# Kernel optimization log

Measured on AMD Instinct MI355X. Metric: run time of the kernel, lower is better.

## Reference

```python
import jax, jax.numpy as jnp
import numpy as np

N = 50000      # nodes
E = 400000     # edges
CIN = 15
HID = 128
HEADS = 4
NC = 2
EPS_BN = 1e-5


def _bn(x, g, b, m, v):
    # BatchNorm1d in eval mode: running stats
    return g * (x - m) * jax.lax.rsqrt(v + EPS_BN) + b


def _gat(x, src, dst, w, a_s, a_d, bias):
    # PyG GATConv(heads=4, concat=False): adds self-loops, per-head attention,
    # softmax over incoming edges (grouped by dst), mean over heads + bias.
    sl = jnp.arange(N, dtype=src.dtype)
    src = jnp.concatenate([src, sl]); dst = jnp.concatenate([dst, sl])
    h = (x @ w).reshape(N, HEADS, HID)                     # [N,H,C]
    a_src = jnp.einsum('nhc,hc->nh', h, a_s)               # [N,H]
    a_dst = jnp.einsum('nhc,hc->nh', h, a_d)
    e = jax.nn.leaky_relu(a_src[src] + a_dst[dst], 0.2)    # [E',H]
    m = jax.ops.segment_max(e, dst, num_segments=N)        # stable segment softmax
    ex = jnp.exp(e - m[dst])
    s = jax.ops.segment_sum(ex, dst, num_segments=N)
    alpha = ex / (s[dst] + 1e-16)
    out = jax.ops.segment_sum(alpha[:, :, None] * h[src], dst, num_segments=N)
    return out.mean(axis=1) + bias                         # concat=False -> head mean


def _gcn(x, src, dst, ew, w, bias):
    # PyG GCNConv with edge_weight: self-loops (weight 1), symmetric normalization.
    sl = jnp.arange(N, dtype=src.dtype)
    src_f = jnp.concatenate([src, sl]); dst_f = jnp.concatenate([dst, sl])
    ew_f = jnp.concatenate([ew, jnp.ones((N,), ew.dtype)])
    deg = jax.ops.segment_sum(ew_f, dst_f, num_segments=N)
    dinv = jnp.where(deg > 0, jax.lax.rsqrt(jnp.maximum(deg, 1e-12)), 0.0)
    norm = dinv[src_f] * ew_f * dinv[dst_f]
    h = x @ w
    return jax.ops.segment_sum(norm[:, None] * h[src_f], dst_f, num_segments=N) + bias


def setup_inputs() -> dict:
    key = jax.random.key(0)
    ks = iter(jax.random.split(key, 40))
    nrm = lambda s, sc: jax.random.normal(next(ks), s, jnp.float32) * sc
    H2 = HID // 2
    inp = {
        'x': jax.random.normal(next(ks), (N, CIN), jnp.float32),
        'edge_index': jax.random.randint(next(ks), (2, E), 0, N, jnp.int32),
        'edge_attr': jax.random.uniform(next(ks), (E, 1), jnp.float32),
        # GATConv params
        'w_gat': nrm((CIN, HEADS * HID), 0.25),
        'att_src': nrm((HEADS, HID), 0.1),
        'att_dst': nrm((HEADS, HID), 0.1),
        'b_gat': jnp.zeros((HID,), jnp.float32),
        # GCNConv params
        'w2': nrm((HID, HID), 0.09), 'b2': jnp.zeros((HID,), jnp.float32),
        'w3': nrm((HID, HID), 0.09), 'b3': jnp.zeros((HID,), jnp.float32),
        'w4': nrm((HID, HID), 0.09), 'b4': jnp.zeros((HID,), jnp.float32),
        # BatchNorm (4 layers stacked): gamma, beta, running_mean, running_var
        'bn_g': 1.0 + nrm((4, HID), 0.1),
        'bn_b': nrm((4, HID), 0.1),
        'bn_m': nrm((4, HID), 0.1),
        'bn_v': 1.0 + 0.1 * jax.random.uniform(next(ks), (4, HID), jnp.float32),
        # dense heads
        'w_shared': nrm((HID, HID), 0.09), 'b_shared': jnp.zeros((HID,), jnp.float32),
        'w_mask1': nrm((HID, H2), 0.09), 'b_mask1': jnp.zeros((H2,), jnp.float32),
        'w_mask2': nrm((H2, NC), 0.12), 'b_mask2': jnp.zeros((NC,), jnp.float32),
        'w_inst1': nrm((HID, H2), 0.09), 'b_inst1': jnp.zeros((H2,), jnp.float32),
        'w_inst2': nrm((H2, NC), 0.12), 'b_inst2': jnp.zeros((NC,), jnp.float32),
        'w_edge1': nrm((HID, H2), 0.09), 'b_edge1': jnp.zeros((H2,), jnp.float32),
        'w_edge2': nrm((H2, 1), 0.12), 'b_edge2': jnp.zeros((1,), jnp.float32),
    }
    return inp


def reference(x, edge_index, edge_attr, w_gat, att_src, att_dst, b_gat,
              w2, b2, w3, b3, w4, b4, bn_g, bn_b, bn_m, bn_v,
              w_shared, b_shared, w_mask1, b_mask1, w_mask2, b_mask2,
              w_inst1, b_inst1, w_inst2, b_inst2, w_edge1, b_edge1, w_edge2, b_edge2):
    src, dst = edge_index[0], edge_index[1]
    ew = edge_attr.squeeze(-1)
    h = jax.nn.relu(_bn(_gat(x, src, dst, w_gat, att_src, att_dst, b_gat),
                        bn_g[0], bn_b[0], bn_m[0], bn_v[0]))
    h = jax.nn.relu(_bn(_gcn(h, src, dst, ew, w2, b2), bn_g[1], bn_b[1], bn_m[1], bn_v[1]))
    h = jax.nn.relu(_bn(_gcn(h, src, dst, ew, w3, b3), bn_g[2], bn_b[2], bn_m[2], bn_v[2]))
    h = jax.nn.relu(_bn(_gcn(h, src, dst, ew, w4, b4), bn_g[3], bn_b[3], bn_m[3], bn_v[3]))
    hs = jax.nn.relu(h @ w_shared + b_shared)
    hm = jax.nn.relu(hs @ w_mask1 + b_mask1)
    mask_out = hm @ w_mask2 + b_mask2
    hi = jax.nn.relu(hs @ w_inst1 + b_inst1)
    instance_out = hi @ w_inst2 + b_inst2
    he = jax.nn.relu(hs @ w_edge1 + b_edge1)
    edge_out = he @ w_edge2 + b_edge2
    return (mask_out, instance_out, edge_out)
```

## Files before the change

kernel.cpp:

```cpp
#include <hip/hip_runtime.h>
#include <hip/hip_bf16.h>

#define NNODES 50000
#define NEDGES 400000
#define ETOT   (NEDGES + NNODES)
#define CIN    15
#define HID    128
#define HEADS  4
#define EPS_BN 1e-5f
#define NB_SCAN ((NNODES + 255) / 256)

typedef __attribute__((ext_vector_type(8))) short bf16x8_t;
typedef __attribute__((ext_vector_type(4))) float f32x4_t;

__device__ __forceinline__ float bfu(unsigned short u) {
  return __uint_as_float(((unsigned)u) << 16);
}
__device__ __forceinline__ unsigned short f2bf(float x) {
  union { __hip_bfloat16 b; unsigned short u; } c;
  c.b = __float2bfloat16(x);
  return c.u;
}
__device__ __forceinline__ float lrelu02(float x) {
  return x > 0.0f ? x : 0.2f * x;
}

template <int WPT, int KT, int ROWS, int FUSEH>
__global__ __launch_bounds__(256) void gemm_mfma_kernel(
    const float* __restrict__ A, const unsigned short* __restrict__ WTh,
    const unsigned short* __restrict__ WTl, const float* __restrict__ bias,
    const float* __restrict__ bg, const float* __restrict__ bb,
    const float* __restrict__ bm, const float* __restrict__ bv,
    void* __restrict__ Cout, int act, int obf16,
    const float* __restrict__ w_m2, const float* __restrict__ b_m2,
    const float* __restrict__ w_i2, const float* __restrict__ b_i2,
    const float* __restrict__ w_e2, const float* __restrict__ b_e2) {
  constexpr int NC = WPT * 64;
  constexpr int RT = ROWS / 16;
  constexpr int CST = NC + 4;
  constexpr int CPR = KT / 8;
  constexpr int ABYTES = ROWS * KT * 2 * 2;
  constexpr int CBYTES = ROWS * CST * 4;
  constexpr int SBYTES = (ABYTES > CBYTES) ? ABYTES : CBYTES;
  __shared__ __align__(16) char smem[SBYTES];
  unsigned short* Ah = (unsigned short*)smem;
  unsigned short* Al = Ah + ROWS * KT;
  float* Cs = (float*)smem;

  const int tid = threadIdx.x;
  const int bm_ = blockIdx.x * ROWS;
  const int wv = tid >> 6, l = tid & 63;
  const int lcol = l & 15;
  const int kg = (l >> 4) << 3;
  const int colbase = wv * (WPT * 16);

#pragma unroll
  for (int i = 0; i < (ROWS * CPR) / 256; ++i) {
    int cch = tid + 256 * i;
    int r = cch / CPR, k0 = (cch % CPR) << 3;
    int gr = bm_ + r;
    float v[8];
    if (gr < NNODES) {
      float4 v0 = *(const float4*)&A[(size_t)gr * KT + k0];
      float4 v1 = *(const float4*)&A[(size_t)gr * KT + k0 + 4];
      v[0] = v0.x; v[1] = v0.y; v[2] = v0.z; v[3] = v0.w;
      v[4] = v1.x; v[5] = v1.y; v[6] = v1.z; v[7] = v1.w;
    } else {
#pragma unroll
      for (int j = 0; j < 8; ++j) v[j] = 0.0f;
    }
    bf16x8_t hv, lv;
#pragma unroll
    for (int j = 0; j < 8; ++j) {
      unsigned short h = f2bf(v[j]);
      hv[j] = (short)h;
      lv[j] = (short)f2bf(v[j] - bfu(h));
    }
    int byte = (k0 << 1) ^ ((r & 7) << 4);
    *(bf16x8_t*)((char*)(Ah + r * KT) + byte) = hv;
    *(bf16x8_t*)((char*)(Al + r * KT) + byte) = lv;
  }
  __syncthreads();

  f32x4_t acc[RT][WPT];
#pragma unroll
  for (int rt = 0; rt < RT; ++rt)
#pragma unroll
    for (int jj = 0; jj < WPT; ++jj) acc[rt][jj] = (f32x4_t){0.f, 0.f, 0.f, 0.f};

#pragma unroll
  for (int kc = 0; kc < KT / 32; ++kc) {
    bf16x8_t cbh[WPT], cbl[WPT];
#pragma unroll
    for (int jj = 0; jj < WPT; ++jj) {
      size_t boff = (size_t)(colbase + jj * 16 + lcol) * KT + kc * 32 + kg;
      cbh[jj] = *(const bf16x8_t*)(WTh + boff);
      cbl[jj] = *(const bf16x8_t*)(WTl + boff);
    }
    int k = kc * 32 + kg;
#pragma unroll
    for (int rt = 0; rt < RT; ++rt) {
      int lrow = rt * 16 + (l & 15);
      int byte = (k << 1) ^ ((lrow & 7) << 4);
      bf16x8_t ah = *(const bf16x8_t*)((const char*)(Ah + lrow * KT) + byte);
      bf16x8_t al = *(const bf16x8_t*)((const char*)(Al + lrow * KT) + byte);
#pragma unroll
      for (int jj = 0; jj < WPT; ++jj) {
        acc[rt][jj] = __builtin_amdgcn_mfma_f32_16x16x32_bf16(ah, cbh[jj], acc[rt][jj], 0, 0, 0);
        acc[rt][jj] = __builtin_amdgcn_mfma_f32_16x16x32_bf16(ah, cbl[jj], acc[rt][jj], 0, 0, 0);
        acc[rt][jj] = __builtin_amdgcn_mfma_f32_16x16x32_bf16(al, cbh[jj], acc[rt][jj], 0, 0, 0);
      }
    }
  }

  __syncthreads();
#pragma unroll
  for (int rt = 0; rt < RT; ++rt) {
    int trow0 = rt * 16 + ((l >> 4) << 2);
#pragma unroll
    for (int jj = 0; jj < WPT; ++jj) {
      int col = colbase + jj * 16 + lcol;
      float bs = bias ? bias[col] : 0.0f;
#pragma unroll
      for (int r = 0; r < 4; ++r) {
        float vv = acc[rt][jj][r] + bs;
        if (bg) vv = bg[col] * (vv - bm[col]) * rsqrtf(bv[col] + EPS_BN) + bb[col];
        if (act) vv = fmaxf(vv, 0.0f);
        Cs[(trow0 + r) * CST + col] = vv;
      }
    }
  }
  __syncthreads();

  if (FUSEH) {
    int r = tid >> 2, q = tid & 3;
    int grow = bm_ + r;
    const float* row = &Cs[r * CST];
    float p0 = 0.f, p1 = 0.f, p2 = 0.f, p3 = 0.f, p4 = 0.f;
#pragma unroll
    for (int e = 0; e < 16; ++e) {
      int c = q * 16 + e;
      float hm = row[c], hi = row[64 + c], he = row[128 + c];
      p0 += hm * w_m2[c * 2 + 0];
      p1 += hm * w_m2[c * 2 + 1];
      p2 += hi * w_i2[c * 2 + 0];
      p3 += hi * w_i2[c * 2 + 1];
      p4 += he * w_e2[c];
    }
#pragma unroll
    for (int off = 1; off < 4; off <<= 1) {
      p0 += __shfl_xor(p0, off);
      p1 += __shfl_xor(p1, off);
      p2 += __shfl_xor(p2, off);
      p3 += __shfl_xor(p3, off);
      p4 += __shfl_xor(p4, off);
    }
    if (q == 0 && grow < NNODES) {
      float* out = (float*)Cout;
      out[grow * 2 + 0] = p0 + b_m2[0];
      out[grow * 2 + 1] = p1 + b_m2[1];
      out[2 * NNODES + grow * 2 + 0] = p2 + b_i2[0];
      out[2 * NNODES + grow * 2 + 1] = p3 + b_i2[1];
      out[4 * NNODES + grow] = p4 + b_e2[0];
    }
  } else {
    constexpr int NJ = (ROWS * NC) / 1024;
#pragma unroll
    for (int j = 0; j < NJ; ++j) {
      int f = tid * 4 + j * 1024;
      int r = f / NC, c = f - r * NC;
      int grow = bm_ + r;
      if (grow >= NNODES) continue;
      float4 v = *(const float4*)&Cs[r * CST + c];
      if (obf16) {
        ushort4 us;
        us.x = f2bf(v.x); us.y = f2bf(v.y); us.z = f2bf(v.z); us.w = f2bf(v.w);
        *(ushort4*)&((unsigned short*)Cout)[(size_t)grow * NC + c] = us;
      } else {
        *(float4*)&((float*)Cout)[(size_t)grow * NC + c] = v;
      }
    }
  }
}

__global__ void prep_att_kernel(const float* __restrict__ w,
                                const float* __restrict__ att_s,
                                const float* __restrict__ att_d,
                                float* __restrict__ wv_s,
                                float* __restrict__ wv_d) {
  int t = threadIdx.x;
  if (t >= 60) return;
  int k = t / 4, h = t & 3;
  float s = 0.f, d = 0.f;
  for (int c = 0; c < 128; ++c) {
    float wk = w[(size_t)k * 512 + h * 128 + c];
    s += wk * att_s[h * 128 + c];
    d += wk * att_d[h * 128 + c];
  }
  wv_s[k * 4 + h] = s;
  wv_d[k * 4 + h] = d;
}

__global__ void pack_wtp_kernel(const float* __restrict__ w,
                                unsigned short* __restrict__ WTh,
                                unsigned short* __restrict__ WTl) {
  int i = blockIdx.x * blockDim.x + threadIdx.x;
  if (i >= 128 * 64) return;
  int c = i >> 6, j = i & 63;
  float xv = 0.f;
  if (j < 60) {
    int h = j / 15, k = j - h * 15;
    xv = 0.25f * w[(size_t)k * 512 + h * 128 + c];
  }
  unsigned short hh = f2bf(xv);
  WTh[i] = hh;
  WTl[i] = f2bf(xv - bfu(hh));
}

__global__ __launch_bounds__(256) void a_sd_kernel(
    const float* __restrict__ x, const float* __restrict__ wv_s,
    const float* __restrict__ wv_d, float* __restrict__ a_s,
    float* __restrict__ a_d) {
  __shared__ float xs[256 * 15];
  __shared__ float wvs[60], wvd[60];
  int t = threadIdx.x;
  int base = blockIdx.x * 256;
  if (t < 60) { wvs[t] = wv_s[t]; wvd[t] = wv_d[t]; }
  for (int i = t; i < 256 * 15; i += 256) {
    int gi = base * 15 + i;
    xs[i] = (gi < NNODES * 15) ? x[gi] : 0.0f;
  }
  __syncthreads();
  int n = base + t;
  if (n >= NNODES) return;
  float a0 = 0, a1 = 0, a2 = 0, a3 = 0, d0 = 0, d1 = 0, d2 = 0, d3 = 0;
#pragma unroll
  for (int k = 0; k < 15; ++k) {
    float xv = xs[t * 15 + k];
    a0 += xv * wvs[k * 4 + 0]; a1 += xv * wvs[k * 4 + 1];
    a2 += xv * wvs[k * 4 + 2]; a3 += xv * wvs[k * 4 + 3];
    d0 += xv * wvd[k * 4 + 0]; d1 += xv * wvd[k * 4 + 1];
    d2 += xv * wvd[k * 4 + 2]; d3 += xv * wvd[k * 4 + 3];
  }
  float4 A; A.x = a0; A.y = a1; A.z = a2; A.w = a3;
  float4 D; D.x = d0; D.y = d1; D.z = d2; D.w = d3;
  *(float4*)&a_s[n * 4] = A;
  *(float4*)&a_d[n * 4] = D;
}

__global__ __launch_bounds__(256) void gat_fused_kernel(
    const float* __restrict__ x, const float* __restrict__ a_s,
    const float* __restrict__ a_d, const int* __restrict__ rowptr,
    const int* __restrict__ csr_src, float* __restrict__ g) {
  int wid = threadIdx.x >> 6, lane = threadIdx.x & 63;
  int n = blockIdx.x * 4 + wid;
  if (n >= NNODES) return;
  int e0 = rowptr[n], e1 = rowptr[n + 1];
  bool on = lane < 60;
  int h = on ? (lane / 15) : 0;
  int k = on ? (lane - h * 15) : 0;
  float adn = a_d[n * 4 + h];

  float ssum = 0.f, acc = 0.f;
  int e = e0;
  for (; e + 4 <= e1; e += 4) {
    int s0 = csr_src[e + 0], s1 = csr_src[e + 1];
    int s2 = csr_src[e + 2], s3 = csr_src[e + 3];
    float as0 = a_s[s0 * 4 + h], as1 = a_s[s1 * 4 + h];
    float as2 = a_s[s2 * 4 + h], as3 = a_s[s3 * 4 + h];
    float x0 = x[(size_t)s0 * CIN + k], x1 = x[(size_t)s1 * CIN + k];
    float x2 = x[(size_t)s2 * CIN + k], x3 = x[(size_t)s3 * CIN + k];
    float ex0 = __expf(lrelu02(as0 + adn));
    float ex1 = __expf(lrelu02(as1 + adn));
    float ex2 = __expf(lrelu02(as2 + adn));
    float ex3 = __expf(lrelu02(as3 + adn));
    ssum += (ex0 + ex1) + (ex2 + ex3);
    acc += ex0 * x0 + ex1 * x1 + ex2 * x2 + ex3 * x3;
  }
  for (; e < e1; ++e) {
    int s = csr_src[e];
    float ex = __expf(lrelu02(a_s[s * 4 + h] + adn));
    ssum += ex;
    acc += ex * x[(size_t)s * CIN + k];
  }
  g[(size_t)n * 64 + lane] = on ? acc / (ssum + 1e-16f) : 0.0f;
}

__global__ void pack_wt4_kernel(
    const float* __restrict__ w2, const float* __restrict__ w3,
    const float* __restrict__ w4, const float* __restrict__ ws,
    unsigned short* __restrict__ Hbase, unsigned short* __restrict__ Lbase) {
  int i = blockIdx.x * blockDim.x + threadIdx.x;
  if (i >= 128 * 128) return;
  const float* W = (blockIdx.y == 0) ? w2 : (blockIdx.y == 1) ? w3
                 : (blockIdx.y == 2) ? w4 : ws;
  unsigned short* Wh = Hbase + (size_t)blockIdx.y * 128 * 128;
  unsigned short* Wl = Lbase + (size_t)blockIdx.y * 128 * 128;
  int k = i >> 7, n = i & 127;
  float x = W[i];
  unsigned short h = f2bf(x);
  Wh[n * 128 + k] = h;
  Wl[n * 128 + k] = f2bf(x - bfu(h));
}

__global__ void pack_wt192_kernel(
    const float* __restrict__ w_m1, const float* __restrict__ w_i1,
    const float* __restrict__ w_e1, const float* __restrict__ b_m1,
    const float* __restrict__ b_i1, const float* __restrict__ b_e1,
    unsigned short* __restrict__ WTh, unsigned short* __restrict__ WTl,
    float* __restrict__ b192) {
  int i = blockIdx.x * blockDim.x + threadIdx.x;
  if (i < 192 * 128) {
    int n = i >> 7, k = i & 127;
    float x = (n < 64) ? w_m1[k * 64 + n]
            : (n < 128) ? w_i1[k * 64 + (n - 64)]
                        : w_e1[k * 64 + (n - 128)];
    unsigned short h = f2bf(x);
    WTh[(size_t)n * 128 + k] = h;
    WTl[(size_t)n * 128 + k] = f2bf(x - bfu(h));
  }
  if (i < 192) {
    b192[i] = (i < 64) ? b_m1[i] : (i < 128) ? b_i1[i - 64] : b_e1[i - 128];
  }
}

__global__ void count_deg_kernel(const int* __restrict__ ei,
                                 const float* __restrict__ ea,
                                 int* __restrict__ cnt,
                                 float* __restrict__ deg) {
  int i = blockIdx.x * blockDim.x + threadIdx.x;
  if (i >= ETOT) return;
  int d; float w;
  if (i < NEDGES) { d = ei[NEDGES + i]; w = ea[i]; }
  else            { d = i - NEDGES; w = 1.0f; }
  atomicAdd(&cnt[d], 1);
  atomicAdd(&deg[d], w);
}

__global__ __launch_bounds__(256) void csr_reduce_kernel(
    const int* __restrict__ cnt, int* __restrict__ bsum) {
  __shared__ int red[256];
  int t = threadIdx.x;
  int i = blockIdx.x * 256 + t;
  red[t] = (i < NNODES) ? cnt[i] : 0;
  __syncthreads();
  for (int off = 128; off > 0; off >>= 1) {
    if (t < off) red[t] += red[t + off];
    __syncthreads();
  }
  if (t == 0) bsum[blockIdx.x] = red[0];
}

__global__ __launch_bounds__(256) void csr_scanb_kernel(
    const int* __restrict__ bsum, int* __restrict__ boff) {
  __shared__ int s[256];
  int t = threadIdx.x;
  s[t] = (t < NB_SCAN) ? bsum[t] : 0;
  __syncthreads();
  for (int off = 1; off < 256; off <<= 1) {
    int u = (t >= off) ? s[t - off] : 0;
    __syncthreads();
    s[t] += u;
    __syncthreads();
  }
  if (t < NB_SCAN) boff[t] = (t == 0) ? 0 : s[t - 1];
}

__global__ __launch_bounds__(256) void csr_scan_kernel(
    int* __restrict__ cnt, const int* __restrict__ boff,
    int* __restrict__ rowptr) {
  __shared__ int s[256];
  int t = threadIdx.x;
  int i = blockIdx.x * 256 + t;
  int v = (i < NNODES) ? cnt[i] : 0;
  s[t] = v;
  __syncthreads();
  for (int off = 1; off < 256; off <<= 1) {
    int u = (t >= off) ? s[t - off] : 0;
    __syncthreads();
    s[t] += u;
    __syncthreads();
  }
  if (i < NNODES) {
    rowptr[i] = boff[blockIdx.x] + s[t] - v;
    cnt[i] = 0;
  }
  if (i == 0) rowptr[NNODES] = ETOT;
}

__global__ void dinv_kernel(const float* __restrict__ deg,
                            float* __restrict__ dinv) {
  int n = blockIdx.x * blockDim.x + threadIdx.x;
  if (n >= NNODES) return;
  float s = deg[n];
  dinv[n] = (s > 0.0f) ? rsqrtf(fmaxf(s, 1e-12f)) : 0.0f;
}

__global__ void scatter_kernel(const int* __restrict__ ei,
                               const float* __restrict__ ea,
                               const float* __restrict__ dinv,
                               const int* __restrict__ rowptr,
                               int* __restrict__ cursor,
                               int* __restrict__ csr_src,
                               float* __restrict__ csr_ew) {
  int i = blockIdx.x * blockDim.x + threadIdx.x;
  if (i >= ETOT) return;
  int s, d; float w;
  if (i < NEDGES) { s = ei[i]; d = ei[NEDGES + i]; w = ea[i]; }
  else            { s = d = i - NEDGES; w = 1.0f; }
  int pos = rowptr[d] + atomicAdd(&cursor[d], 1);
  csr_src[pos] = s;
  csr_ew[pos] = dinv[s] * w * dinv[d];
}

__global__ __launch_bounds__(256) void gcn_gather_kernel(
    const __hip_bfloat16* __restrict__ h, const int* __restrict__ rowptr,
    const int* __restrict__ csr_src, const float* __restrict__ csr_w,
    const float* __restrict__ bias,
    const float* __restrict__ bg, const float* __restrict__ bb,
    const float* __restrict__ bm, const float* __restrict__ bv,
    float* __restrict__ out) {
  int wid = threadIdx.x >> 6, lane = threadIdx.x & 63;
  int n = blockIdx.x * 4 + wid;
  if (n >= NNODES) return;
  int e0 = rowptr[n], e1 = rowptr[n + 1];
  int c = 2 * lane;
  float ax = 0.f, ay = 0.f;
  int e = e0;
  for (; e + 4 <= e1; e += 4) {
    int s0 = csr_src[e + 0], s1 = csr_src[e + 1];
    int s2 = csr_src[e + 2], s3 = csr_src[e + 3];
    float w0 = csr_w[e + 0], w1 = csr_w[e + 1];
    float w2 = csr_w[e + 2], w3 = csr_w[e + 3];
    ushort2 u0 = *(const ushort2*)(h + (size_t)s0 * HID + c);
    ushort2 u1 = *(const ushort2*)(h + (size_t)s1 * HID + c);
    ushort2 u2 = *(const ushort2*)(h + (size_t)s2 * HID + c);
    ushort2 u3 = *(const ushort2*)(h + (size_t)s3 * HID + c);
    ax += w0 * bfu(u0.x) + w1 * bfu(u1.x) + w2 * bfu(u2.x) + w3 * bfu(u3.x);
    ay += w0 * bfu(u0.y) + w1 * bfu(u1.y) + w2 * bfu(u2.y) + w3 * bfu(u3.y);
  }
  for (; e < e1; ++e) {
    int s = csr_src[e];
    float w = csr_w[e];
    ushort2 u = *(const ushort2*)(h + (size_t)s * HID + c);
    ax += w * bfu(u.x);
    ay += w * bfu(u.y);
  }
  float ox = ax + bias[c];
  float oy = ay + bias[c + 1];
  ox = bg[c] * (ox - bm[c]) * rsqrtf(bv[c] + EPS_BN) + bb[c];
  oy = bg[c + 1] * (oy - bm[c + 1]) * rsqrtf(bv[c + 1] + EPS_BN) + bb[c + 1];
  ox = fmaxf(ox, 0.0f); oy = fmaxf(oy, 0.0f);
  float2 o; o.x = ox; o.y = oy;
  *(float2*)&out[(size_t)n * HID + c] = o;
}

extern "C" void kernel_launch(void* const* d_in, const int* in_sizes, int n_in,
                              void* d_out, int out_size, void* d_ws, size_t ws_size,
                              hipStream_t stream) {
  const float* x       = (const float*)d_in[0];
  const int*   ei      = (const int*)d_in[1];
  const float* ea      = (const float*)d_in[2];
  const float* w_gat   = (const float*)d_in[3];
  const float* att_src = (const float*)d_in[4];
  const float* att_dst = (const float*)d_in[5];
  const float* b_gat   = (const float*)d_in[6];
  const float* w2 = (const float*)d_in[7];  const float* b2 = (const float*)d_in[8];
  const float* w3 = (const float*)d_in[9];  const float* b3 = (const float*)d_in[10];
  const float* w4 = (const float*)d_in[11]; const float* b4 = (const float*)d_in[12];
  const float* bn_g = (const float*)d_in[13];
  const float* bn_b = (const float*)d_in[14];
  const float* bn_m = (const float*)d_in[15];
  const float* bn_v = (const float*)d_in[16];
  const float* w_shared = (const float*)d_in[17]; const float* b_shared = (const float*)d_in[18];
  const float* w_m1 = (const float*)d_in[19]; const float* b_m1 = (const float*)d_in[20];
  const float* w_m2 = (const float*)d_in[21]; const float* b_m2 = (const float*)d_in[22];
  const float* w_i1 = (const float*)d_in[23]; const float* b_i1 = (const float*)d_in[24];
  const float* w_i2 = (const float*)d_in[25]; const float* b_i2 = (const float*)d_in[26];
  const float* w_e1 = (const float*)d_in[27]; const float* b_e1 = (const float*)d_in[28];
  const float* w_e2 = (const float*)d_in[29]; const float* b_e2 = (const float*)d_in[30];
  float* out = (float*)d_out;

  size_t off = 0;
  auto alloc = [&](size_t bytes) -> char* {
    char* p = (char*)d_ws + off;
    off += (bytes + 255) & ~(size_t)255;
    return p;
  };
  float* p0      = (float*)alloc((size_t)NNODES * HID * 4);
  float* p1      = (float*)alloc((size_t)NNODES * HID * 4);
  float* g       = (float*)alloc((size_t)NNODES * 64 * 4);
  __hip_bfloat16* hb = (__hip_bfloat16*)alloc((size_t)NNODES * HID * 2);
  float* a_s     = (float*)alloc((size_t)NNODES * 4 * 4);
  float* a_d     = (float*)alloc((size_t)NNODES * 4 * 4);
  float* deg     = (float*)alloc((size_t)NNODES * 4);
  float* dinv    = (float*)alloc((size_t)NNODES * 4);
  float* csr_ew  = (float*)alloc((size_t)ETOT * 4);
  int*   rowptr  = (int*)alloc((size_t)(NNODES + 1) * 4);
  int*   cnt     = (int*)alloc((size_t)NNODES * 4);
  int*   csr_src = (int*)alloc((size_t)ETOT * 4);
  int*   bsum    = (int*)alloc((size_t)NB_SCAN * 4);
  int*   boff    = (int*)alloc((size_t)NB_SCAN * 4);
  unsigned short* wtH = (unsigned short*)alloc(4 * 128 * 128 * 2);
  unsigned short* wtL = (unsigned short*)alloc(4 * 128 * 128 * 2);
  unsigned short* wt192h = (unsigned short*)alloc(192 * 128 * 2);
  unsigned short* wt192l = (unsigned short*)alloc(192 * 128 * 2);
  unsigned short* wtph = (unsigned short*)alloc(128 * 64 * 2);
  unsigned short* wtpl = (unsigned short*)alloc(128 * 64 * 2);
  float* b192 = (float*)alloc(192 * 4);
  float* wv_s = (float*)alloc(60 * 4);
  float* wv_d = (float*)alloc(60 * 4);

  unsigned short* wt2h = wtH + 0 * 16384; unsigned short* wt2l = wtL + 0 * 16384;
  unsigned short* wt3h = wtH + 1 * 16384; unsigned short* wt3l = wtL + 1 * 16384;
  unsigned short* wt4h = wtH + 2 * 16384; unsigned short* wt4l = wtL + 2 * 16384;
  unsigned short* wsh  = wtH + 3 * 16384; unsigned short* wsl  = wtL + 3 * 16384;

  dim3 blk256(256);
  dim3 wgrid((NNODES + 3) / 4);
  dim3 mgrid((NNODES + 63) / 64);

  hipMemsetAsync(cnt, 0, NNODES * 4, stream);
  hipMemsetAsync(deg, 0, NNODES * 4, stream);
  count_deg_kernel<<<(ETOT + 255) / 256, blk256, 0, stream>>>(ei, ea, cnt, deg);
  csr_reduce_kernel<<<NB_SCAN, blk256, 0, stream>>>(cnt, bsum);
  csr_scanb_kernel<<<1, blk256, 0, stream>>>(bsum, boff);
  csr_scan_kernel<<<NB_SCAN, blk256, 0, stream>>>(cnt, boff, rowptr);
  dinv_kernel<<<(NNODES + 255) / 256, blk256, 0, stream>>>(deg, dinv);
  scatter_kernel<<<(ETOT + 255) / 256, blk256, 0, stream>>>(
      ei, ea, dinv, rowptr, cnt, csr_src, csr_ew);

  prep_att_kernel<<<1, 64, 0, stream>>>(w_gat, att_src, att_dst, wv_s, wv_d);
  pack_wtp_kernel<<<(128 * 64 + 255) / 256, blk256, 0, stream>>>(w_gat, wtph, wtpl);
  pack_wt4_kernel<<<dim3((128 * 128 + 255) / 256, 4), blk256, 0, stream>>>(
      w2, w3, w4, w_shared, wtH, wtL);
  pack_wt192_kernel<<<(192 * 128 + 255) / 256, blk256, 0, stream>>>(
      w_m1, w_i1, w_e1, b_m1, b_i1, b_e1, wt192h, wt192l, b192);

  a_sd_kernel<<<NB_SCAN, blk256, 0, stream>>>(x, wv_s, wv_d, a_s, a_d);

  gat_fused_kernel<<<wgrid, blk256, 0, stream>>>(
      x, a_s, a_d, rowptr, csr_src, g);

  gemm_mfma_kernel<2, 64, 64, 0><<<mgrid, blk256, 0, stream>>>(
      g, wtph, wtpl, b_gat, bn_g + 0, bn_b + 0, bn_m + 0, bn_v + 0, p0, 1, 0,
      nullptr, nullptr, nullptr, nullptr, nullptr, nullptr);

  gemm_mfma_kernel<2, 128, 64, 0><<<mgrid, blk256, 0, stream>>>(
      p0, wt2h, wt2l, nullptr, nullptr, nullptr, nullptr, nullptr, hb, 0, 1,
      nullptr, nullptr, nullptr, nullptr, nullptr, nullptr);
  gcn_gather_kernel<<<wgrid, blk256, 0, stream>>>(
      hb, rowptr, csr_src, csr_ew, b2,
      bn_g + 128, bn_b + 128, bn_m + 128, bn_v + 128, p1);

  gemm_mfma_kernel<2, 128, 64, 0><<<mgrid, blk256, 0, stream>>>(
      p1, wt3h, wt3l, nullptr, nullptr, nullptr, nullptr, nullptr, hb, 0, 1,
      nullptr, nullptr, nullptr, nullptr, nullptr, nullptr);
  gcn_gather_kernel<<<wgrid, blk256, 0, stream>>>(
      hb, rowptr, csr_src, csr_ew, b3,
      bn_g + 256, bn_b + 256, bn_m + 256, bn_v + 256, p0);

  gemm_mfma_kernel<2, 128, 64, 0><<<mgrid, blk256, 0, stream>>>(
      p0, wt4h, wt4l, nullptr, nullptr, nullptr, nullptr, nullptr, hb, 0, 1,
      nullptr, nullptr, nullptr, nullptr, nullptr, nullptr);
  gcn_gather_kernel<<<wgrid, blk256, 0, stream>>>(
      hb, rowptr, csr_src, csr_ew, b4,
      bn_g + 384, bn_b + 384, bn_m + 384, bn_v + 384, p1);

  gemm_mfma_kernel<2, 128, 64, 0><<<mgrid, blk256, 0, stream>>>(
      p1, wsh, wsl, b_shared, nullptr, nullptr, nullptr, nullptr, p0, 1, 0,
      nullptr, nullptr, nullptr, nullptr, nullptr, nullptr);

  gemm_mfma_kernel<3, 128, 64, 1><<<mgrid, blk256, 0, stream>>>(
      p0, wt192h, wt192l, b192, nullptr, nullptr, nullptr, nullptr, out, 1, 0,
      w_m2, b_m2, w_i2, b_i2, w_e2, b_e2);
}
```

Baseline: 334.1 us.

## Store activations pre-split into bf16 hi/lo planes, load GEMM A directly

Producers (GAT aggregation, GCN gather, GEMM epilogues) now write activations as two bf16 planes (high and residual) instead of fp32. The GEMM reads its A fragments straight from global memory in MFMA layout, removing the LDS staging, the per-block fp32-to-bf16 split and one barrier. Activation buffers are padded to a multiple of 64 rows so the unguarded loads stay in bounds. Padded rows are never written, so the GEMM reads uninitialised data there, although those rows are never stored. Global A loads are less coalesced than the old LDS path and may be re-fetched across the four waves.

```diff
diff --git a/kernel.cpp b/kernel.cpp
--- a/kernel.cpp
+++ b/kernel.cpp
@@ -2,6 +2,7 @@
 #include <hip/hip_bf16.h>
 
 #define NNODES 50000
+#define NPAD   50048
 #define NEDGES 400000
 #define ETOT   (NEDGES + NNODES)
 #define CIN    15
@@ -25,66 +26,31 @@
   return x > 0.0f ? x : 0.2f * x;
 }
 
-template <int WPT, int KT, int ROWS, int FUSEH>
+template <int WPT, int KT, int FUSEH>
 __global__ __launch_bounds__(256) void gemm_mfma_kernel(
-    const float* __restrict__ A, const unsigned short* __restrict__ WTh,
-    const unsigned short* __restrict__ WTl, const float* __restrict__ bias,
+    const unsigned short* __restrict__ Ahg, const unsigned short* __restrict__ Alg,
+    const unsigned short* __restrict__ WTh, const unsigned short* __restrict__ WTl,
+    const float* __restrict__ bias,
     const float* __restrict__ bg, const float* __restrict__ bb,
     const float* __restrict__ bm, const float* __restrict__ bv,
-    void* __restrict__ Cout, int act, int obf16,
+    void* __restrict__ CoutA, void* __restrict__ CoutB, int act, int omode,
     const float* __restrict__ w_m2, const float* __restrict__ b_m2,
     const float* __restrict__ w_i2, const float* __restrict__ b_i2,
     const float* __restrict__ w_e2, const float* __restrict__ b_e2) {
   constexpr int NC = WPT * 64;
-  constexpr int RT = ROWS / 16;
   constexpr int CST = NC + 4;
-  constexpr int CPR = KT / 8;
-  constexpr int ABYTES = ROWS * KT * 2 * 2;
-  constexpr int CBYTES = ROWS * CST * 4;
-  constexpr int SBYTES = (ABYTES > CBYTES) ? ABYTES : CBYTES;
-  __shared__ __align__(16) char smem[SBYTES];
-  unsigned short* Ah = (unsigned short*)smem;
-  unsigned short* Al = Ah + ROWS * KT;
-  float* Cs = (float*)smem;
+  __shared__ __align__(16) float Cs[64 * CST];
 
   const int tid = threadIdx.x;
-  const int bm_ = blockIdx.x * ROWS;
+  const int bm_ = blockIdx.x * 64;
   const int wv = tid >> 6, l = tid & 63;
   const int lcol = l & 15;
   const int kg = (l >> 4) << 3;
   const int colbase = wv * (WPT * 16);
 
-#pragma unroll
-  for (int i = 0; i < (ROWS * CPR) / 256; ++i) {
-    int cch = tid + 256 * i;
-    int r = cch / CPR, k0 = (cch % CPR) << 3;
-    int gr = bm_ + r;
-    float v[8];
-    if (gr < NNODES) {
-      float4 v0 = *(const float4*)&A[(size_t)gr * KT + k0];
-      float4 v1 = *(const float4*)&A[(size_t)gr * KT + k0 + 4];
-      v[0] = v0.x; v[1] = v0.y; v[2] = v0.z; v[3] = v0.w;
-      v[4] = v1.x; v[5] = v1.y; v[6] = v1.z; v[7] = v1.w;
-    } else {
-#pragma unroll
-      for (int j = 0; j < 8; ++j) v[j] = 0.0f;
-    }
-    bf16x8_t hv, lv;
-#pragma unroll
-    for (int j = 0; j < 8; ++j) {
-      unsigned short h = f2bf(v[j]);
-      hv[j] = (short)h;
-      lv[j] = (short)f2bf(v[j] - bfu(h));
-    }
-    int byte = (k0 << 1) ^ ((r & 7) << 4);
-    *(bf16x8_t*)((char*)(Ah + r * KT) + byte) = hv;
-    *(bf16x8_t*)((char*)(Al + r * KT) + byte) = lv;
-  }
-  __syncthreads();
-
-  f32x4_t acc[RT][WPT];
-#pragma unroll
-  for (int rt = 0; rt < RT; ++rt)
+  f32x4_t acc[4][WPT];
+#pragma unroll
+  for (int rt = 0; rt < 4; ++rt)
 #pragma unroll
     for (int jj = 0; jj < WPT; ++jj) acc[rt][jj] = (f32x4_t){0.f, 0.f, 0.f, 0.f};
 
@@ -97,13 +63,11 @@
       cbh[jj] = *(const bf16x8_t*)(WTh + boff);
       cbl[jj] = *(const bf16x8_t*)(WTl + boff);
     }
-    int k = kc * 32 + kg;
-#pragma unroll
-    for (int rt = 0; rt < RT; ++rt) {
-      int lrow = rt * 16 + (l & 15);
-      int byte = (k << 1) ^ ((lrow & 7) << 4);
-      bf16x8_t ah = *(const bf16x8_t*)((const char*)(Ah + lrow * KT) + byte);
-      bf16x8_t al = *(const bf16x8_t*)((const char*)(Al + lrow * KT) + byte);
+#pragma unroll
+    for (int rt = 0; rt < 4; ++rt) {
+      size_t aoff = (size_t)(bm_ + rt * 16 + (l & 15)) * KT + kc * 32 + kg;
+      bf16x8_t ah = *(const bf16x8_t*)(Ahg + aoff);
+      bf16x8_t al = *(const bf16x8_t*)(Alg + aoff);
 #pragma unroll
       for (int jj = 0; jj < WPT; ++jj) {
         acc[rt][jj] = __builtin_amdgcn_mfma_f32_16x16x32_bf16(ah, cbh[jj], acc[rt][jj], 0, 0, 0);
@@ -113,9 +77,8 @@
     }
   }
 
-  __syncthreads();
-#pragma unroll
-  for (int rt = 0; rt < RT; ++rt) {
+#pragma unroll
+  for (int rt = 0; rt < 4; ++rt) {
     int trow0 = rt * 16 + ((l >> 4) << 2);
 #pragma unroll
     for (int jj = 0; jj < WPT; ++jj) {
@@ -156,7 +119,7 @@
       p4 += __shfl_xor(p4, off);
     }
     if (q == 0 && grow < NNODES) {
-      float* out = (float*)Cout;
+      float* out = (float*)CoutA;
       out[grow * 2 + 0] = p0 + b_m2[0];
       out[grow * 2 + 1] = p1 + b_m2[1];
       out[2 * NNODES + grow * 2 + 0] = p2 + b_i2[0];
@@ -164,7 +127,7 @@
       out[4 * NNODES + grow] = p4 + b_e2[0];
     }
   } else {
-    constexpr int NJ = (ROWS * NC) / 1024;
+    constexpr int NJ = (64 * NC) / 1024;
 #pragma unroll
     for (int j = 0; j < NJ; ++j) {
       int f = tid * 4 + j * 1024;
@@ -172,12 +135,16 @@
       int grow = bm_ + r;
       if (grow >= NNODES) continue;
       float4 v = *(const float4*)&Cs[r * CST + c];
-      if (obf16) {
-        ushort4 us;
-        us.x = f2bf(v.x); us.y = f2bf(v.y); us.z = f2bf(v.z); us.w = f2bf(v.w);
-        *(ushort4*)&((unsigned short*)Cout)[(size_t)grow * NC + c] = us;
-      } else {
-        *(float4*)&((float*)Cout)[(size_t)grow * NC + c] = v;
+      ushort4 hi4;
+      hi4.x = f2bf(v.x); hi4.y = f2bf(v.y); hi4.z = f2bf(v.z); hi4.w = f2bf(v.w);
+      *(ushort4*)&((unsigned short*)CoutA)[(size_t)grow * NC + c] = hi4;
+      if (omode == 2) {
+        ushort4 lo4;
+        lo4.x = f2bf(v.x - bfu(hi4.x));
+        lo4.y = f2bf(v.y - bfu(hi4.y));
+        lo4.z = f2bf(v.z - bfu(hi4.z));
+        lo4.w = f2bf(v.w - bfu(hi4.w));
+        *(ushort4*)&((unsigned short*)CoutB)[(size_t)grow * NC + c] = lo4;
       }
     }
   }
@@ -251,7 +218,8 @@
 __global__ __launch_bounds__(256) void gat_fused_kernel(
     const float* __restrict__ x, const float* __restrict__ a_s,
     const float* __restrict__ a_d, const int* __restrict__ rowptr,
-    const int* __restrict__ csr_src, float* __restrict__ g) {
+    const int* __restrict__ csr_src, unsigned short* __restrict__ gh,
+    unsigned short* __restrict__ gl) {
   int wid = threadIdx.x >> 6, lane = threadIdx.x & 63;
   int n = blockIdx.x * 4 + wid;
   if (n >= NNODES) return;
@@ -283,7 +251,10 @@
     ssum += ex;
     acc += ex * x[(size_t)s * CIN + k];
   }
-  g[(size_t)n * 64 + lane] = on ? acc / (ssum + 1e-16f) : 0.0f;
+  float v = on ? acc / (ssum + 1e-16f) : 0.0f;
+  unsigned short hv = f2bf(v);
+  gh[(size_t)n * 64 + lane] = hv;
+  gl[(size_t)n * 64 + lane] = f2bf(v - bfu(hv));
 }
 
 __global__ void pack_wt4_kernel(
@@ -419,7 +390,7 @@
     const float* __restrict__ bias,
     const float* __restrict__ bg, const float* __restrict__ bb,
     const float* __restrict__ bm, const float* __restrict__ bv,
-    float* __restrict__ out) {
+    unsigned short* __restrict__ outh, unsigned short* __restrict__ outl) {
   int wid = threadIdx.x >> 6, lane = threadIdx.x & 63;
   int n = blockIdx.x * 4 + wid;
   if (n >= NNODES) return;
@@ -451,8 +422,12 @@
   ox = bg[c] * (ox - bm[c]) * rsqrtf(bv[c] + EPS_BN) + bb[c];
   oy = bg[c + 1] * (oy - bm[c + 1]) * rsqrtf(bv[c + 1] + EPS_BN) + bb[c + 1];
   ox = fmaxf(ox, 0.0f); oy = fmaxf(oy, 0.0f);
-  float2 o; o.x = ox; o.y = oy;
-  *(float2*)&out[(size_t)n * HID + c] = o;
+  ushort2 hi2, lo2;
+  hi2.x = f2bf(ox); hi2.y = f2bf(oy);
+  lo2.x = f2bf(ox - bfu(hi2.x));
+  lo2.y = f2bf(oy - bfu(hi2.y));
+  *(ushort2*)&outh[(size_t)n * HID + c] = hi2;
+  *(ushort2*)&outl[(size_t)n * HID + c] = lo2;
 }
 
 extern "C" void kernel_launch(void* const* d_in, const int* in_sizes, int n_in,
@@ -487,10 +462,13 @@
     off += (bytes + 255) & ~(size_t)255;
     return p;
   };
-  float* p0      = (float*)alloc((size_t)NNODES * HID * 4);
-  float* p1      = (float*)alloc((size_t)NNODES * HID * 4);
-  float* g       = (float*)alloc((size_t)NNODES * 64 * 4);
-  __hip_bfloat16* hb = (__hip_bfloat16*)alloc((size_t)NNODES * HID * 2);
+  unsigned short* p0h = (unsigned short*)alloc((size_t)NPAD * HID * 2);
+  unsigned short* p0l = (unsigned short*)alloc((size_t)NPAD * HID * 2);
+  unsigned short* p1h = (unsigned short*)alloc((size_t)NPAD * HID * 2);
+  unsigned short* p1l = (unsigned short*)alloc((size_t)NPAD * HID * 2);
+  unsigned short* gh  = (unsigned short*)alloc((size_t)NPAD * 64 * 2);
+  unsigned short* gl  = (unsigned short*)alloc((size_t)NPAD * 64 * 2);
+  __hip_bfloat16* hb  = (__hip_bfloat16*)alloc((size_t)NPAD * HID * 2);
   float* a_s     = (float*)alloc((size_t)NNODES * 4 * 4);
   float* a_d     = (float*)alloc((size_t)NNODES * 4 * 4);
   float* deg     = (float*)alloc((size_t)NNODES * 4);
@@ -540,38 +518,38 @@
   a_sd_kernel<<<NB_SCAN, blk256, 0, stream>>>(x, wv_s, wv_d, a_s, a_d);
 
   gat_fused_kernel<<<wgrid, blk256, 0, stream>>>(
-      x, a_s, a_d, rowptr, csr_src, g);
-
-  gemm_mfma_kernel<2, 64, 64, 0><<<mgrid, blk256, 0, stream>>>(
-      g, wtph, wtpl, b_gat, bn_g + 0, bn_b + 0, bn_m + 0, bn_v + 0, p0, 1, 0,
-      nullptr, nullptr, nullptr, nullptr, nullptr, nullptr);
-
-  gemm_mfma_kernel<2, 128, 64, 0><<<mgrid, blk256, 0, stream>>>(
-      p0, wt2h, wt2l, nullptr, nullptr, nullptr, nullptr, nullptr, hb, 0, 1,
-      nullptr, nullptr, nullptr, nullptr, nullptr, nullptr);
+      x, a_s, a_d, rowptr, csr_src, gh, gl);
+
+  gemm_mfma_kernel<2, 64, 0><<<mgrid, blk256, 0, stream>>>(
+      gh, gl, wtph, wtpl, b_gat, bn_g + 0, bn_b + 0, bn_m + 0, bn_v + 0,
+      p0h, p0l, 1, 2, nullptr, nullptr, nullptr, nullptr, nullptr, nullptr);
+
+  gemm_mfma_kernel<2, 128, 0><<<mgrid, blk256, 0, stream>>>(
+      p0h, p0l, wt2h, wt2l, nullptr, nullptr, nullptr, nullptr, nullptr,
+      hb, nullptr, 0, 1, nullptr, nullptr, nullptr, nullptr, nullptr, nullptr);
   gcn_gather_kernel<<<wgrid, blk256, 0, stream>>>(
       hb, rowptr, csr_src, csr_ew, b2,
-      bn_g + 128, bn_b + 128, bn_m + 128, bn_v + 128, p1);
-
-  gemm_mfma_kernel<2, 128, 64, 0><<<mgrid, blk256, 0, stream>>>(
-      p1, wt3h, wt3l, nullptr, nullptr, nullptr, nullptr, nullptr, hb, 0, 1,
-      nullptr, nullptr, nullptr, nullptr, nullptr, nullptr);
+      bn_g + 128, bn_b + 128, bn_m + 128, bn_v + 128, p1h, p1l);
+
+  gemm_mfma_kernel<2, 128, 0><<<mgrid, blk256, 0, stream>>>(
+      p1h, p1l, wt3h, wt3l, nullptr, nullptr, nullptr, nullptr, nullptr,
+      hb, nullptr, 0, 1, nullptr, nullptr, nullptr, nullptr, nullptr, nullptr);
   gcn_gather_kernel<<<wgrid, blk256, 0, stream>>>(
       hb, rowptr, csr_src, csr_ew, b3,
-      bn_g + 256, bn_b + 256, bn_m + 256, bn_v + 256, p0);
-
-  gemm_mfma_kernel<2, 128, 64, 0><<<mgrid, blk256, 0, stream>>>(
-      p0, wt4h, wt4l, nullptr, nullptr, nullptr, nullptr, nullptr, hb, 0, 1,
-      nullptr, nullptr, nullptr, nullptr, nullptr, nullptr);
+      bn_g + 256, bn_b + 256, bn_m + 256, bn_v + 256, p0h, p0l);
+
+  gemm_mfma_kernel<2, 128, 0><<<mgrid, blk256, 0, stream>>>(
+      p0h, p0l, wt4h, wt4l, nullptr, nullptr, nullptr, nullptr, nullptr,
+      hb, nullptr, 0, 1, nullptr, nullptr, nullptr, nullptr, nullptr, nullptr);
   gcn_gather_kernel<<<wgrid, blk256, 0, stream>>>(
       hb, rowptr, csr_src, csr_ew, b4,
-      bn_g + 384, bn_b + 384, bn_m + 384, bn_v + 384, p1);
-
-  gemm_mfma_kernel<2, 128, 64, 0><<<mgrid, blk256, 0, stream>>>(
-      p1, wsh, wsl, b_shared, nullptr, nullptr, nullptr, nullptr, p0, 1, 0,
-      nullptr, nullptr, nullptr, nullptr, nullptr, nullptr);
-
-  gemm_mfma_kernel<3, 128, 64, 1><<<mgrid, blk256, 0, stream>>>(
-      p0, wt192h, wt192l, b192, nullptr, nullptr, nullptr, nullptr, out, 1, 0,
-      w_m2, b_m2, w_i2, b_i2, w_e2, b_e2);
-}
+      bn_g + 384, bn_b + 384, bn_m + 384, bn_v + 384, p1h, p1l);
+
+  gemm_mfma_kernel<2, 128, 0><<<mgrid, blk256, 0, stream>>>(
+      p1h, p1l, wsh, wsl, b_shared, nullptr, nullptr, nullptr, nullptr,
+      p0h, p0l, 1, 2, nullptr, nullptr, nullptr, nullptr, nullptr, nullptr);
+
+  gemm_mfma_kernel<3, 128, 1><<<mgrid, blk256, 0, stream>>>(
+      p0h, p0l, wt192h, wt192l, b192, nullptr, nullptr, nullptr, nullptr,
+      out, nullptr, 1, 0, w_m2, b_m2, w_i2, b_i2, w_e2, b_e2);
+}
```

Result: slower. 390.7 us (+17.0%).
